# Kernel optimization log

Hardware: AMD Instinct MI355X
Metric: run time of the kernel (lower is better)

The kernel has to match this reference:

```python
import jax, jax.numpy as jnp
import numpy as np

N_NODES = 50000
N_EDGES = 800000
IN_DIM = 128
OUT_DIM = 64
NEG_SLOPE = 0.01  # torch F.leaky_relu default


def setup_inputs() -> dict:
    key = jax.random.key(0)
    ks = jax.random.split(key, 7)
    h = jax.random.normal(ks[0], (N_NODES, IN_DIM), dtype=jnp.float32)
    embed = jax.random.uniform(ks[1], (N_EDGES, 1), dtype=jnp.float32)
    src = jax.random.randint(ks[2], (N_EDGES,), 0, N_NODES)
    dst = jax.random.randint(ks[3], (N_EDGES,), 0, N_NODES)
    # parameters (Linear weights, no bias); stored as [in, out] for x @ W
    W_fc = jax.random.normal(ks[4], (IN_DIM, OUT_DIM), dtype=jnp.float32) / np.sqrt(IN_DIM)
    W_attn = jax.random.normal(ks[5], (3 * OUT_DIM, 1), dtype=jnp.float32) / np.sqrt(3 * OUT_DIM)
    W_feat = jax.random.normal(ks[6], (1, OUT_DIM), dtype=jnp.float32)
    return {"h": h, "embed": embed, "src": src, "dst": dst,
            "W_fc": W_fc, "W_attn": W_attn, "W_feat": W_feat}


def reference(h, embed, src, dst, W_fc, W_attn, W_feat):
    n = h.shape[0]
    z = h @ W_fc                                  # [N, D]
    # split attn weight so we never materialize the [E, 3D] concat
    Wa_src, Wa_dst, Wa_feat = jnp.split(W_attn, 3, axis=0)  # each [D, 1]
    a_src = (z @ Wa_src)[:, 0]                    # [N]
    a_dst = (z @ Wa_dst)[:, 0]                    # [N]
    dfeat = embed @ W_feat                        # [E, D]
    e = a_src[src] + a_dst[dst] + (dfeat @ Wa_feat)[:, 0]  # [E]
    e = jnp.where(e >= 0, e, NEG_SLOPE * e)       # leaky_relu
    # segment softmax over incoming edges of each dst node
    seg_max = jax.ops.segment_max(e, dst, num_segments=n)  # [N]
    ex = jnp.exp(e - seg_max[dst])                # [E]
    denom = jax.ops.segment_sum(ex, dst, num_segments=n)   # [N]
    alpha = ex / denom[dst]                       # [E]
    # weighted scatter-sum of source features
    out = jax.ops.segment_sum(alpha[:, None] * z[src], dst, num_segments=n)  # [N, D]
    return out
```

## Files before the change

kernel.cpp:

```cpp
#include <hip/hip_runtime.h>
#include <hip/hip_fp16.h>

#define N_NODES 50000
#define N_EDGES 800000
#define IN_DIM 128
#define OUT_DIM 64
#define NEG_SLOPE 0.01f

#define BUCK_SHIFT 6
#define BUCK_NODES 64
#define NBUCK ((N_NODES + BUCK_NODES - 1) / BUCK_NODES)
#define CAP 1536
#define EPB 4096
#define NBLK_SCAT ((N_EDGES + EPB - 1) / EPB)

typedef unsigned int uint;

__device__ __forceinline__ unsigned short f2h(float x) {
    return __half_as_ushort(__float2half_rn(x));
}
__device__ __forceinline__ float h2f(unsigned short u) {
    return __half2float(__ushort_as_half(u));
}

__launch_bounds__(256)
__global__ void k_fc(const float* __restrict__ h,
                     const float* __restrict__ W_fc,
                     const float* __restrict__ W_attn,
                     const float* __restrict__ W_feat,
                     uint* __restrict__ z16, float* __restrict__ a_src, float* __restrict__ a_dst,
                     int* __restrict__ gcursor, float* __restrict__ c_ws) {
    __shared__ float Wlds[IN_DIM * OUT_DIM];
    const float4* Wg = (const float4*)W_fc;
    float4* Wl = (float4*)Wlds;
    #pragma unroll
    for (int i = 0; i < 8; ++i) Wl[threadIdx.x + i * 256] = Wg[threadIdx.x + i * 256];

    int g = blockIdx.x * 256 + threadIdx.x;
    if (g < NBUCK) gcursor[g] = g * CAP;
    if (blockIdx.x == 0 && threadIdx.x < 64) {
        int lane = threadIdx.x;
        float p = W_feat[lane] * W_attn[128 + lane];
        #pragma unroll
        for (int off = 32; off; off >>= 1) p += __shfl_xor(p, off, 64);
        if (lane == 0) c_ws[0] = p;
    }
    __syncthreads();

    int n = g >> 2;
    int q = g & 3;
    if (n >= N_NODES) return;

    float acc[16];
    #pragma unroll
    for (int i = 0; i < 16; ++i) acc[i] = 0.f;

    const float4* hrow = (const float4*)(h + (size_t)n * IN_DIM);

    for (int kc = 0; kc < IN_DIM / 4; ++kc) {
        float4 hv = hrow[kc];
        #pragma unroll
        for (int j = 0; j < 4; ++j) {
            float hk = (j == 0) ? hv.x : (j == 1) ? hv.y : (j == 2) ? hv.z : hv.w;
            const float4* Wr = (const float4*)Wlds + (kc * 4 + j) * (OUT_DIM / 4) + q * 4;
            #pragma unroll
            for (int i = 0; i < 4; ++i) {
                float4 wv = Wr[i];
                acc[i * 4 + 0] += hk * wv.x;
                acc[i * 4 + 1] += hk * wv.y;
                acc[i * 4 + 2] += hk * wv.z;
                acc[i * 4 + 3] += hk * wv.w;
            }
        }
    }

    uint* zrow = z16 + (size_t)n * (OUT_DIM / 2) + q * 8;
    #pragma unroll
    for (int i = 0; i < 8; ++i)
        zrow[i] = (uint)f2h(acc[2 * i]) | ((uint)f2h(acc[2 * i + 1]) << 16);

    const float* wa_s = W_attn + q * 16;
    const float* wa_d = W_attn + OUT_DIM + q * 16;
    float ps = 0.f, pd = 0.f;
    #pragma unroll
    for (int i = 0; i < 16; ++i) { ps += acc[i] * wa_s[i]; pd += acc[i] * wa_d[i]; }
    ps += __shfl_xor(ps, 1, 64); ps += __shfl_xor(ps, 2, 64);
    pd += __shfl_xor(pd, 1, 64); pd += __shfl_xor(pd, 2, 64);
    if (q == 0) { a_src[n] = ps; a_dst[n] = pd; }
}

__launch_bounds__(1024)
__global__ void k_binscat(const int* __restrict__ src, const int* __restrict__ dst,
                          const float* __restrict__ embed,
                          const float* __restrict__ a_src, const float* __restrict__ a_dst,
                          const float* __restrict__ c_ws,
                          int* __restrict__ gcursor, uint2* __restrict__ entries) {
    __shared__ uint2 s_ent[EPB];
    __shared__ int hist[NBUCK];
    __shared__ int boff[NBUCK];
    int t = threadIdx.x;
    if (t < NBUCK) hist[t] = 0;
    __syncthreads();

    int e0 = blockIdx.x * EPB;
    int e1 = e0 + EPB; if (e1 > N_EDGES) e1 = N_EDGES;
    int m = e1 - e0;
    float cc = c_ws[0];

    for (int i = t; i < m; i += 1024) {
        int e = e0 + i;
        int s = src[e], d = dst[e];
        float ev = a_src[s] + a_dst[d] + cc * embed[e];
        ev = (ev >= 0.f) ? ev : NEG_SLOPE * ev;
        float ex = __expf(ev);
        uint b = (uint)d >> BUCK_SHIFT, dl = (uint)d & (BUCK_NODES - 1);
        s_ent[i] = make_uint2((uint)s | (dl << 16) | (b << 22), __float_as_uint(ex));
        atomicAdd(&hist[b], 1);
    }
    __syncthreads();

    if (t < NBUCK) {
        int c = hist[t];
        boff[t] = c ? atomicAdd(&gcursor[t], c) : 0;
        hist[t] = 0;
    }
    __syncthreads();

    for (int i = t; i < m; i += 1024) {
        uint2 p = s_ent[i];
        uint b = p.x >> 22;
        int pos = boff[b] + atomicAdd(&hist[b], 1);
        entries[pos] = make_uint2(p.x & 0x3FFFFFu, p.y);
    }
}

__launch_bounds__(512)
__global__ void k_gather(const int* __restrict__ gcursor, const uint2* __restrict__ entries,
                         const uint* __restrict__ z16, float* __restrict__ out) {
    __shared__ uint2 s_stash[CAP];
    __shared__ uint  s_pk2[CAP];
    __shared__ int hist[BUCK_NODES], hoff[BUCK_NODES], hcur[BUCK_NODES];

    int b = blockIdx.x;
    int t = threadIdx.x, lane = t & 63, wid = t >> 6;
    int base = b * CAP;
    int m = gcursor[b] - base;
    if (m > CAP) m = CAP;

    if (t < BUCK_NODES) hist[t] = 0;
    __syncthreads();

    for (int i = t; i < m; i += 512) {
        uint2 p = entries[base + i];
        s_stash[i] = p;
        atomicAdd(&hist[(p.x >> 16) & 63], 1);
    }
    __syncthreads();

    if (wid == 0) {
        int v = hist[lane], sc = v;
        #pragma unroll
        for (int off = 1; off < 64; off <<= 1) {
            int u = __shfl_up(sc, off, 64);
            if (lane >= off) sc += u;
        }
        hoff[lane] = sc - v;
        hcur[lane] = sc - v;
    }
    __syncthreads();

    for (int i = t; i < m; i += 512) {
        uint2 p = s_stash[i];
        int pos = atomicAdd(&hcur[(p.x >> 16) & 63], 1);
        s_pk2[pos] = (p.x & 0xFFFFu) | ((uint)f2h(__uint_as_float(p.y)) << 16);
    }
    __syncthreads();

    int half = lane >> 5, dp = lane & 31;
    for (int k = 0; k < 8; ++k) {
        int dl = wid * 8 + k;
        int n = b * BUCK_NODES + dl;
        if (n >= N_NODES) continue;
        int j0 = hoff[dl], c = hist[dl], j1 = j0 + c;
        float accx = 0.f, accy = 0.f, den = 0.f;
        for (int j = j0; j < j1; j += 16) {
            uint pk[8];
            #pragma unroll
            for (int u = 0; u < 8; ++u) {
                int idx = j + 8 * half + u;
                int idc = (idx < j1) ? idx : (j1 - 1);
                pk[u] = s_pk2[idc];
                if (idx >= j1) pk[u] &= 0xFFFFu;
            }
            uint zv[8];
            #pragma unroll
            for (int u = 0; u < 8; ++u) zv[u] = z16[(size_t)(pk[u] & 0xFFFFu) * 32 + dp];
            #pragma unroll
            for (int u = 0; u < 8; ++u) {
                float ex = h2f((unsigned short)(pk[u] >> 16));
                den  += ex;
                accx += ex * h2f((unsigned short)(zv[u] & 0xFFFFu));
                accy += ex * h2f((unsigned short)(zv[u] >> 16));
            }
        }
        accx += __shfl_xor(accx, 32, 64);
        accy += __shfl_xor(accy, 32, 64);
        den  += __shfl_xor(den, 32, 64);
        if (lane < 32) {
            float2 r = (c > 0) ? make_float2(accx / den, accy / den) : make_float2(0.f, 0.f);
            ((float2*)(out + (size_t)n * OUT_DIM))[dp] = r;
        }
    }
}

extern "C" void kernel_launch(void* const* d_in, const int* in_sizes, int n_in,
                              void* d_out, int out_size, void* d_ws, size_t ws_size,
                              hipStream_t stream) {
    const float* h      = (const float*)d_in[0];
    const float* embed  = (const float*)d_in[1];
    const int*   src    = (const int*)d_in[2];
    const int*   dst    = (const int*)d_in[3];
    const float* W_fc   = (const float*)d_in[4];
    const float* W_attn = (const float*)d_in[5];
    const float* W_feat = (const float*)d_in[6];

    float* ws      = (float*)d_ws;
    uint*  z16     = (uint*)ws;
    uint2* entries = (uint2*)(z16 + (size_t)N_NODES * 32);
    float* a_src   = (float*)(entries + (size_t)NBUCK * CAP);
    float* a_dst   = a_src + N_NODES;
    float* c_ws    = a_dst + N_NODES;
    int*   gcursor = (int*)(c_ws + 1);

    float* out = (float*)d_out;

    k_fc<<<(N_NODES * 4 + 255) / 256, 256, 0, stream>>>(h, W_fc, W_attn, W_feat,
                                                        z16, a_src, a_dst, gcursor, c_ws);
    k_binscat<<<NBLK_SCAT, 1024, 0, stream>>>(src, dst, embed, a_src, a_dst, c_ws,
                                              gcursor, entries);
    k_gather<<<NBUCK, 512, 0, stream>>>(gcursor, entries, z16, out);
}
```

Before: 77.00 us.

## Move a_dst lookup and exp into gather kernel, vectorize binscat edge loads

Binscat no longer does a random gather of a_dst per edge. It stores a partial score (a_src plus the embed term). Gather loads the 64 a_dst values for its bucket into shared memory and finishes the leaky_relu and exp there. Binscat also reads src, dst and embed as int4/float4, four edges per thread. This removes one random global read per edge, in exchange for a bit more ALU work in the gather's reorder pass.

New measurement: 74.69 us. 3.0% less time.

```diff
diff --git a/kernel.cpp b/kernel.cpp
--- a/kernel.cpp
+++ b/kernel.cpp
@@ -92,7 +92,7 @@
 __launch_bounds__(1024)
 __global__ void k_binscat(const int* __restrict__ src, const int* __restrict__ dst,
                           const float* __restrict__ embed,
-                          const float* __restrict__ a_src, const float* __restrict__ a_dst,
+                          const float* __restrict__ a_src,
                           const float* __restrict__ c_ws,
                           int* __restrict__ gcursor, uint2* __restrict__ entries) {
     __shared__ uint2 s_ent[EPB];
@@ -107,15 +107,32 @@
     int m = e1 - e0;
     float cc = c_ws[0];
 
-    for (int i = t; i < m; i += 1024) {
-        int e = e0 + i;
-        int s = src[e], d = dst[e];
-        float ev = a_src[s] + a_dst[d] + cc * embed[e];
-        ev = (ev >= 0.f) ? ev : NEG_SLOPE * ev;
-        float ex = __expf(ev);
-        uint b = (uint)d >> BUCK_SHIFT, dl = (uint)d & (BUCK_NODES - 1);
-        s_ent[i] = make_uint2((uint)s | (dl << 16) | (b << 22), __float_as_uint(ex));
-        atomicAdd(&hist[b], 1);
+    int i0 = t * 4;
+    if (i0 + 3 < m) {
+        int4   s4 = ((const int4*)(src + e0))[t];
+        int4   d4 = ((const int4*)(dst + e0))[t];
+        float4 m4 = ((const float4*)(embed + e0))[t];
+        int    ss[4] = {s4.x, s4.y, s4.z, s4.w};
+        int    dd[4] = {d4.x, d4.y, d4.z, d4.w};
+        float  mm[4] = {m4.x, m4.y, m4.z, m4.w};
+        #pragma unroll
+        for (int u = 0; u < 4; ++u) {
+            float partial = a_src[ss[u]] + cc * mm[u];
+            uint b = (uint)dd[u] >> BUCK_SHIFT, dl = (uint)dd[u] & (BUCK_NODES - 1);
+            s_ent[i0 + u] = make_uint2((uint)ss[u] | (dl << 16) | (b << 22),
+                                       __float_as_uint(partial));
+            atomicAdd(&hist[b], 1);
+        }
+    } else {
+        for (int i = i0; i < m; ++i) {
+            int e = e0 + i;
+            int s = src[e], d = dst[e];
+            float partial = a_src[s] + cc * embed[e];
+            uint b = (uint)d >> BUCK_SHIFT, dl = (uint)d & (BUCK_NODES - 1);
+            s_ent[i] = make_uint2((uint)s | (dl << 16) | (b << 22),
+                                  __float_as_uint(partial));
+            atomicAdd(&hist[b], 1);
+        }
     }
     __syncthreads();
 
@@ -136,9 +153,11 @@
 
 __launch_bounds__(512)
 __global__ void k_gather(const int* __restrict__ gcursor, const uint2* __restrict__ entries,
+                         const float* __restrict__ a_dst,
                          const uint* __restrict__ z16, float* __restrict__ out) {
     __shared__ uint2 s_stash[CAP];
     __shared__ uint  s_pk2[CAP];
+    __shared__ float s_adst[BUCK_NODES];
     __shared__ int hist[BUCK_NODES], hoff[BUCK_NODES], hcur[BUCK_NODES];
 
     int b = blockIdx.x;
@@ -147,7 +166,11 @@
     int m = gcursor[b] - base;
     if (m > CAP) m = CAP;
 
-    if (t < BUCK_NODES) hist[t] = 0;
+    if (t < BUCK_NODES) {
+        hist[t] = 0;
+        int n = b * BUCK_NODES + t;
+        s_adst[t] = (n < N_NODES) ? a_dst[n] : 0.f;
+    }
     __syncthreads();
 
     for (int i = t; i < m; i += 512) {
@@ -171,8 +194,12 @@
 
     for (int i = t; i < m; i += 512) {
         uint2 p = s_stash[i];
-        int pos = atomicAdd(&hcur[(p.x >> 16) & 63], 1);
-        s_pk2[pos] = (p.x & 0xFFFFu) | ((uint)f2h(__uint_as_float(p.y)) << 16);
+        int dl = (p.x >> 16) & 63;
+        float ev = __uint_as_float(p.y) + s_adst[dl];
+        ev = (ev >= 0.f) ? ev : NEG_SLOPE * ev;
+        float ex = __expf(ev);
+        int pos = atomicAdd(&hcur[dl], 1);
+        s_pk2[pos] = (p.x & 0xFFFFu) | ((uint)f2h(ex) << 16);
     }
     __syncthreads();
 
@@ -236,7 +263,7 @@
 
     k_fc<<<(N_NODES * 4 + 255) / 256, 256, 0, stream>>>(h, W_fc, W_attn, W_feat,
                                                         z16, a_src, a_dst, gcursor, c_ws);
-    k_binscat<<<NBLK_SCAT, 1024, 0, stream>>>(src, dst, embed, a_src, a_dst, c_ws,
+    k_binscat<<<NBLK_SCAT, 1024, 0, stream>>>(src, dst, embed, a_src, c_ws,
                                               gcursor, entries);
-    k_gather<<<NBUCK, 512, 0, stream>>>(gcursor, entries, z16, out);
-}
+    k_gather<<<NBUCK, 512, 0, stream>>>(gcursor, entries, a_dst, z16, out);
+}
```
